# Optimization experiments

Measured on AMD Instinct MI355X. Metric: run time of the kernel, lower is better.

The kernel has to match this reference:

```python
import jax, jax.numpy as jnp
import numpy as np

N_NODES = 100000
N_EDGES = 1600000
IN_DIM, HID, EMB = 128, 128, 128
NUM_EDGE_FEAT = 3
BN_EPS = 1e-5


def _lin(key, fan_in, fan_out):
    k1, k2 = jax.random.split(key)
    lim = 1.0 / np.sqrt(fan_in)
    W = jax.random.uniform(k1, (fan_in, fan_out), minval=-lim, maxval=lim, dtype=jnp.float32)
    b = jax.random.uniform(k2, (fan_out,), minval=-lim, maxval=lim, dtype=jnp.float32)
    return W, b


def setup_inputs() -> dict:
    key = jax.random.key(0)
    ks = jax.random.split(key, 12)
    x = jax.random.normal(ks[0], (N_NODES, IN_DIM), dtype=jnp.float32)
    edge_index = jax.random.randint(ks[1], (2, N_EDGES), 0, N_NODES, dtype=jnp.int32)
    edge_attr = jax.random.normal(ks[2], (N_EDGES, NUM_EDGE_FEAT), dtype=jnp.float32)
    params = {}
    dims = [(IN_DIM, HID), (HID, HID), (HID, HID)]
    for i, (fi, fo) in enumerate(dims, 1):
        W, b = _lin(ks[2 + i], fi, fo)
        We, be = _lin(ks[5 + i], NUM_EDGE_FEAT, fo)
        params[f'W{i}'] = W; params[f'b{i}'] = b
        params[f'We{i}'] = We; params[f'be{i}'] = be
        params[f'g{i}'] = jnp.ones((fo,), jnp.float32)
        params[f'bt{i}'] = jnp.zeros((fo,), jnp.float32)
    Wl, bl = _lin(ks[9], HID, EMB)
    params['Wl'] = Wl; params['bl'] = bl
    return {'x': x, 'edge_index': edge_index, 'edge_attr': edge_attr, **params}


def _gcn_conv(x, row, col, edge_attr, W, b, We, be):
    h = x @ W + b                    # [N, d]
    e = edge_attr @ We + be          # [E, d]
    n = x.shape[0]
    deg = jax.ops.segment_sum(jnp.ones_like(row, dtype=h.dtype), row, num_segments=n) + 1.0
    dinv = deg ** -0.5               # deg >= 1, never inf
    norm = dinv[row] * dinv[col]     # [E]
    msg = norm[:, None] * jax.nn.relu(h[row] + e)  # gather + fused elementwise
    return jax.ops.segment_sum(msg, col, num_segments=n)  # scatter-add to targets


def _bn(x, g, bt):
    m = jnp.mean(x, axis=0)
    v = jnp.mean((x - m) ** 2, axis=0)  # biased var (training-mode batchnorm)
    return (x - m) * jax.lax.rsqrt(v + BN_EPS) * g + bt


def reference(x, edge_index, edge_attr,
              W1, b1, We1, be1, g1, bt1,
              W2, b2, We2, be2, g2, bt2,
              W3, b3, We3, be3, g3, bt3,
              Wl, bl):
    row, col = edge_index[0], edge_index[1]
    h = jax.nn.relu(_gcn_conv(x, row, col, edge_attr, W1, b1, We1, be1))
    h = _bn(h, g1, bt1)
    h = jax.nn.relu(_gcn_conv(h, row, col, edge_attr, W2, b2, We2, be2))
    h = _bn(h, g2, bt2)
    h = jax.nn.relu(_gcn_conv(h, row, col, edge_attr, W3, b3, We3, be3))
    h = _bn(h, g3, bt3)
    return h @ Wl + bl
```

## Files before the change

### kernel.cpp

```cpp
#include <hip/hip_runtime.h>
#include <stdint.h>

#define NN 100000
#define NE 1600000
#define DIM 128
#define BN_EPS 1e-5f
#define NBUCK 391
#define NBLK_GEMM 1563
#define NBLK_AGG 6250
#define NB_HIST 512
#define CSR_PAD 32
#define NREP 64

typedef unsigned int uint;
typedef unsigned short ushort;
typedef unsigned char uchar;
typedef __attribute__((ext_vector_type(8))) short short8;
typedef __attribute__((ext_vector_type(4))) float f32x4;
typedef __attribute__((ext_vector_type(2))) float v2f;


static __device__ __forceinline__ ushort f2bf(float f) {
    uint u = __float_as_uint(f);
    u += 0x7FFF + ((u >> 16) & 1);
    return (ushort)(u >> 16);
}
static __device__ __forceinline__ float bf_lo(uint p) { return __uint_as_float(p << 16); }
static __device__ __forceinline__ float bf_hi(uint p) { return __uint_as_float(p & 0xFFFF0000u); }

static __device__ __forceinline__ v2f vfma(v2f a, v2f b, v2f c) {
    return __builtin_elementwise_fma(a, b, c);
}
static __device__ __forceinline__ v2f vbc(float s) { v2f r = {s, s}; return r; }


__global__ __launch_bounds__(256) void k_count(const int* __restrict__ ei,
                                               int* __restrict__ rowCnt,
                                               int* __restrict__ colCnt) {
    __shared__ int hr[NBUCK], hc[NBUCK];
    int tid = threadIdx.x;
    for (int b = tid; b < NBUCK; b += 256) { hr[b] = 0; hc[b] = 0; }
    __syncthreads();
    const int gstep = NB_HIST * 256;
    const int gt = blockIdx.x * 256 + tid;
    for (int e = gt; e < NE; e += gstep) {
        atomicAdd(&hr[ei[e] >> 8], 1);
        atomicAdd(&hc[ei[NE + e] >> 8], 1);
    }
    __syncthreads();
    for (int b = tid; b < NBUCK; b += 256) {
        if (hr[b]) atomicAdd(&rowCnt[b], hr[b]);
        if (hc[b]) atomicAdd(&colCnt[b], hc[b]);
    }
}

__global__ __launch_bounds__(512) void k_scanb(const int* __restrict__ rowCnt,
                                               const int* __restrict__ colCnt,
                                               int* __restrict__ rowBase,
                                               int* __restrict__ colBase,
                                               int* __restrict__ rowCur,
                                               int* __restrict__ colCur) {
    __shared__ int s[512];
    int tid = threadIdx.x;
    int v = (tid < NBUCK) ? rowCnt[tid] : 0;
    s[tid] = v;
    __syncthreads();
    for (int d = 1; d < 512; d <<= 1) {
        int a = (tid >= d) ? s[tid - d] : 0;
        __syncthreads();
        s[tid] += a;
        __syncthreads();
    }
    if (tid < NBUCK) { int e = s[tid] - v; rowBase[tid] = e; rowCur[tid] = e; }
    if (tid == NBUCK) rowBase[NBUCK] = s[NBUCK];
    __syncthreads();
    v = (tid < NBUCK) ? colCnt[tid] : 0;
    s[tid] = v;
    __syncthreads();
    for (int d = 1; d < 512; d <<= 1) {
        int a = (tid >= d) ? s[tid - d] : 0;
        __syncthreads();
        s[tid] += a;
        __syncthreads();
    }
    if (tid < NBUCK) { int e = s[tid] - v; colBase[tid] = e; colCur[tid] = e; }
    if (tid == NBUCK) colBase[NBUCK] = s[NBUCK];
}

__global__ __launch_bounds__(256) void k_scat(const int* __restrict__ ei,
                                              const float* __restrict__ ea,
                                              int* __restrict__ rowCur,
                                              int* __restrict__ colCur,
                                              uchar* __restrict__ rowScat,
                                              uint4* __restrict__ tmp) {
    __shared__ int hr[NBUCK], hc[NBUCK], lbr[NBUCK], lbc[NBUCK], lcr[NBUCK], lcc[NBUCK];
    int tid = threadIdx.x;
    for (int b = tid; b < NBUCK; b += 256) { hr[b] = 0; hc[b] = 0; lcr[b] = 0; lcc[b] = 0; }
    __syncthreads();
    const int gstep = NB_HIST * 256;
    const int gt = blockIdx.x * 256 + tid;
    for (int e = gt; e < NE; e += gstep) {
        atomicAdd(&hr[ei[e] >> 8], 1);
        atomicAdd(&hc[ei[NE + e] >> 8], 1);
    }
    __syncthreads();
    for (int b = tid; b < NBUCK; b += 256) {
        lbr[b] = hr[b] ? atomicAdd(&rowCur[b], hr[b]) : 0;
        lbc[b] = hc[b] ? atomicAdd(&colCur[b], hc[b]) : 0;
    }
    __syncthreads();
    for (int e = gt; e < NE; e += gstep) {
        int r = ei[e];
        int c = ei[NE + e];
        int posr = lbr[r >> 8] + atomicAdd(&lcr[r >> 8], 1);
        rowScat[posr] = (uchar)(r & 255);
        float3 eav = *(const float3*)&ea[(size_t)e * 3];
        uint4 rec;
        rec.x = 0u;
        rec.y = ((uint)f2bf(eav.x) << 16) | (uint)f2bf(eav.y);
        rec.z = ((uint)f2bf(eav.z) << 16) | (uint)(c & 255);
        rec.w = (uint)r;
        int posc = lbc[c >> 8] + atomicAdd(&lcc[c >> 8], 1);
        tmp[posc] = rec;
    }
}

__global__ __launch_bounds__(1024) void k_deg(const uchar* __restrict__ rowScat,
                                              const int* __restrict__ rowBase,
                                              float* __restrict__ dinv) {
    __shared__ int h[256];
    int tid = threadIdx.x;
    int b = blockIdx.x;
    if (tid < 256) h[tid] = 0;
    __syncthreads();
    int base = rowBase[b], cnt = rowBase[b + 1] - base;
    for (int i = tid; i < cnt; i += 1024) atomicAdd(&h[rowScat[base + i]], 1);
    __syncthreads();
    if (tid < 256) {
        int node = b * 256 + tid;
        if (node < NN) dinv[node] = rsqrtf((float)h[tid] + 1.0f);
    }
}

__global__ __launch_bounds__(1024) void k_sort_col(const uint4* __restrict__ tmp,
                                                   const int* __restrict__ colBase,
                                                   const float* __restrict__ dinv,
                                                   uint4* __restrict__ csr,
                                                   int* __restrict__ offs) {
    __shared__ int hh[256], sc[256], cur[256];
    __shared__ float dloc[256];
    int tid = threadIdx.x;
    int b = blockIdx.x;
    if (tid < 256) {
        hh[tid] = 0;
        int node = b * 256 + tid;
        dloc[tid] = (node < NN) ? dinv[node] : 0.0f;
    }
    __syncthreads();
    int base = colBase[b], cnt = colBase[b + 1] - base;
    for (int i = tid; i < cnt; i += 1024) atomicAdd(&hh[tmp[base + i].z & 255], 1);
    __syncthreads();
    int v = 0;
    if (tid < 256) { v = hh[tid]; sc[tid] = v; }
    __syncthreads();
    for (int d = 1; d < 256; d <<= 1) {
        int add = 0;
        if (tid < 256 && tid >= d) add = sc[tid - d];
        __syncthreads();
        if (tid < 256) sc[tid] += add;
        __syncthreads();
    }
    if (tid < 256) {
        int excl = sc[tid] - v;
        int node = b * 256 + tid;
        if (node < NN) offs[node] = base + excl;
        if (b == NBUCK - 1 && tid == 0) offs[NN] = NE;
        cur[tid] = excl;
    }
    __syncthreads();
    for (int i = tid; i < cnt; i += 1024) {
        uint4 rec = tmp[base + i];
        int f = rec.z & 255;
        rec.x = __float_as_uint(dinv[(int)rec.w] * dloc[f]);
        int pos = atomicAdd(&cur[f], 1);
        csr[base + pos] = rec;
    }
}


__global__ __launch_bounds__(128) void k_prep(const float* __restrict__ W,
                                              const float* __restrict__ b,
                                              const float* __restrict__ g,
                                              const float* __restrict__ bt,
                                              const float* __restrict__ sprev,
                                              float* __restrict__ snext,
                                              int mode,
                                              ushort* __restrict__ Wt,
                                              float* __restrict__ beff) {
    __shared__ float s[DIM];
    int k = threadIdx.x;
    if (k < 64) snext[blockIdx.x * 64 + k] = 0.0f;
    float A = 1.0f, B = 0.0f;
    if (mode) {
        float sm = 0.0f, sq = 0.0f;
        for (int r = 0; r < NREP; ++r) {
            sm += sprev[r * 256 + k];
            sq += sprev[r * 256 + 128 + k];
        }
        float m = sm * (1.0f / NN);
        float var = sq * (1.0f / NN) - m * m;
        float rs = rsqrtf(var + BN_EPS);
        A = rs * g[k];
        B = bt[k] - m * A;
    }
    if (blockIdx.x < DIM) {
        int n = blockIdx.x;
        Wt[n * DIM + k] = f2bf(A * W[k * DIM + n]);
    } else {
        int j = blockIdx.x - DIM;
        s[k] = B * W[k * DIM + j];
        __syncthreads();
        for (int d = 64; d > 0; d >>= 1) {
            if (k < d) s[k] += s[k + d];
            __syncthreads();
        }
        if (k == 0) beff[j] = b[j] + s[0];
    }
}


#define GEMM_LANE_SETUP                                                             \
    const int lane = threadIdx.x & 63;                                              \
    const int wv   = threadIdx.x >> 6;                                              \
    const int m    = lane & 15;                                                     \
    const int quad = lane >> 4;                                                     \
    const int row0 = blockIdx.x * 64 + wv * 16;                                     \
    const int rr   = min(row0 + m, NN - 1);

#define GEMM_MFMA_CORE(a0, a1, a2, a3, Wt)                                          \
    f32x4 acc[8];                                                                   \
    _Pragma("unroll")                                                               \
    for (int ft = 0; ft < 8; ++ft) {                                                \
        const short8* bp = (const short8*)&Wt[(size_t)(ft * 16 + m) * DIM + quad * 8]; \
        f32x4 c = {0.f, 0.f, 0.f, 0.f};                                             \
        c = __builtin_amdgcn_mfma_f32_16x16x32_bf16(bp[0],  a0, c, 0, 0, 0);        \
        c = __builtin_amdgcn_mfma_f32_16x16x32_bf16(bp[4],  a1, c, 0, 0, 0);        \
        c = __builtin_amdgcn_mfma_f32_16x16x32_bf16(bp[8],  a2, c, 0, 0, 0);        \
        c = __builtin_amdgcn_mfma_f32_16x16x32_bf16(bp[12], a3, c, 0, 0, 0);        \
        acc[ft] = c;                                                                \
    }                                                                               \
    const int node = row0 + m;

#define GEMM_STORE_BF16(Y)                                                          \
    if (node < NN) {                                                                \
        ushort* yp = &Y[(size_t)node * DIM + quad * 4];                             \
        _Pragma("unroll")                                                           \
        for (int ft = 0; ft < 8; ++ft) {                                            \
            float4 bb = *(const float4*)&beff[ft * 16 + quad * 4];                  \
            ushort4 o = {f2bf(acc[ft][0] + bb.x), f2bf(acc[ft][1] + bb.y),          \
                         f2bf(acc[ft][2] + bb.z), f2bf(acc[ft][3] + bb.w)};         \
            *(ushort4*)&yp[ft * 16] = o;                                            \
        }                                                                           \
    }

static __device__ __forceinline__ short8 cvt8(float4 a, float4 b) {
    short8 r;
    r[0] = (short)f2bf(a.x); r[1] = (short)f2bf(a.y);
    r[2] = (short)f2bf(a.z); r[3] = (short)f2bf(a.w);
    r[4] = (short)f2bf(b.x); r[5] = (short)f2bf(b.y);
    r[6] = (short)f2bf(b.z); r[7] = (short)f2bf(b.w);
    return r;
}

__global__ __launch_bounds__(256) void k_gemm_mf_f32in(const float* __restrict__ Af,
                                                       const ushort* __restrict__ Wt,
                                                       const float* __restrict__ beff,
                                                       ushort* __restrict__ Y) {
    GEMM_LANE_SETUP
    const float4* apf = (const float4*)&Af[(size_t)rr * DIM] + quad * 2;
    short8 a0 = cvt8(apf[0],  apf[1]);
    short8 a1 = cvt8(apf[8],  apf[9]);
    short8 a2 = cvt8(apf[16], apf[17]);
    short8 a3 = cvt8(apf[24], apf[25]);
    GEMM_MFMA_CORE(a0, a1, a2, a3, Wt)
    GEMM_STORE_BF16(Y)
}

__global__ __launch_bounds__(256) void k_gemm_mf_bf(const ushort* __restrict__ Abf,
                                                    const ushort* __restrict__ Wt,
                                                    const float* __restrict__ beff,
                                                    ushort* __restrict__ Y) {
    GEMM_LANE_SETUP
    const short8* ap = (const short8*)&Abf[(size_t)rr * DIM + quad * 8];
    short8 a0 = ap[0];
    short8 a1 = ap[4];
    short8 a2 = ap[8];
    short8 a3 = ap[12];
    GEMM_MFMA_CORE(a0, a1, a2, a3, Wt)
    GEMM_STORE_BF16(Y)
}

__global__ __launch_bounds__(256) void k_gemm_mf_f32(const ushort* __restrict__ Abf,
                                                     const ushort* __restrict__ Wt,
                                                     const float* __restrict__ beff,
                                                     float* __restrict__ Y) {
    GEMM_LANE_SETUP
    const short8* ap = (const short8*)&Abf[(size_t)rr * DIM + quad * 8];
    short8 a0 = ap[0];
    short8 a1 = ap[4];
    short8 a2 = ap[8];
    short8 a3 = ap[12];
    GEMM_MFMA_CORE(a0, a1, a2, a3, Wt)
    if (node < NN) {
        float* yp = &Y[(size_t)node * DIM + quad * 4];
#pragma unroll
        for (int ft = 0; ft < 8; ++ft) {
            float4 bb = *(const float4*)&beff[ft * 16 + quad * 4];
            float4 o = {acc[ft][0] + bb.x, acc[ft][1] + bb.y,
                        acc[ft][2] + bb.z, acc[ft][3] + bb.w};
            *(float4*)&yp[ft * 16] = o;
        }
    }
}


static __device__ __forceinline__ void edge_compute(float4 r, float4 hv, float n,
                                                    const v2f* __restrict__ w0,
                                                    const v2f* __restrict__ w1,
                                                    const v2f* __restrict__ w2,
                                                    const v2f* __restrict__ vbe,
                                                    v2f* __restrict__ acc) {
    uint py = __float_as_uint(r.y), pz = __float_as_uint(r.z);
    v2f va0 = vbc(bf_hi(py)), va1 = vbc(bf_lo(py)), va2 = vbc(bf_hi(pz));
    v2f vn = vbc(n);
    uint hx = __float_as_uint(hv.x), hy = __float_as_uint(hv.y);
    uint hz = __float_as_uint(hv.z), hw = __float_as_uint(hv.w);
    v2f hp[4] = {{bf_lo(hx), bf_hi(hx)}, {bf_lo(hy), bf_hi(hy)},
                 {bf_lo(hz), bf_hi(hz)}, {bf_lo(hw), bf_hi(hw)}};
    const v2f z = {0.0f, 0.0f};
#pragma unroll
    for (int j = 0; j < 4; ++j) {
        v2f e = vfma(va2, w2[j], vbe[j]);
        e = vfma(va1, w1[j], e);
        e = vfma(va0, w0[j], e);
        v2f u = hp[j] + e;
        u = __builtin_elementwise_max(u, z);
        acc[j] = vfma(vn, u, acc[j]);
    }
}

__global__ __launch_bounds__(256) void k_agg(const float4* __restrict__ h4,
                                             const float4* __restrict__ csr,
                                             const int* __restrict__ offs,
                                             const float* __restrict__ We,
                                             const float* __restrict__ be,
                                             uint* __restrict__ tb,
                                             float* __restrict__ stats) {
    __shared__ float pbuf[4][256];
    int wv = threadIdx.x >> 6;
    int lane = threadIdx.x & 63;
    int q  = lane >> 4;
    int oc = lane & 15;
    int j0 = oc * 8;

    float4 t0, t1;
    t0 = *(const float4*)&We[j0];             t1 = *(const float4*)&We[j0 + 4];
    v2f w0[4] = {{t0.x, t0.y}, {t0.z, t0.w}, {t1.x, t1.y}, {t1.z, t1.w}};
    t0 = *(const float4*)&We[DIM + j0];       t1 = *(const float4*)&We[DIM + j0 + 4];
    v2f w1[4] = {{t0.x, t0.y}, {t0.z, t0.w}, {t1.x, t1.y}, {t1.z, t1.w}};
    t0 = *(const float4*)&We[2 * DIM + j0];   t1 = *(const float4*)&We[2 * DIM + j0 + 4];
    v2f w2[4] = {{t0.x, t0.y}, {t0.z, t0.w}, {t1.x, t1.y}, {t1.z, t1.w}};
    t0 = *(const float4*)&be[j0];             t1 = *(const float4*)&be[j0 + 4];
    v2f vbe[4] = {{t0.x, t0.y}, {t0.z, t0.w}, {t1.x, t1.y}, {t1.z, t1.w}};

    v2f smv[4] = {{0,0},{0,0},{0,0},{0,0}};
    v2f sqv[4] = {{0,0},{0,0},{0,0},{0,0}};

    const int v0 = blockIdx.x * 16 + wv * 4;
    int ofs[5];
#pragma unroll
    for (int k = 0; k < 5; ++k) ofs[k] = offs[v0 + k];

    for (int it = 0; it < 4; ++it) {
        int v = v0 + it;
        v2f acc[4] = {{0,0},{0,0},{0,0},{0,0}};
        int s0 = ofs[it], e0 = ofs[it + 1];

        float4 rA1 = csr[s0 + q];
        float4 rA2 = csr[s0 + 4 + q];
        float4 rB1 = csr[s0 + 8 + q];
        float4 rB2 = csr[s0 + 12 + q];
        float4 hA1 = h4[(size_t)__float_as_int(rA1.w) * 16 + oc];
        float4 hA2 = h4[(size_t)__float_as_int(rA2.w) * 16 + oc];

#pragma unroll 2
        for (int base = s0; base < e0; base += 8) {
            float4 hB1 = h4[(size_t)__float_as_int(rB1.w) * 16 + oc];
            float4 hB2 = h4[(size_t)__float_as_int(rB2.w) * 16 + oc];
            float4 rC1 = csr[base + 16 + q];
            float4 rC2 = csr[base + 20 + q];
            float n1 = (base + q < e0) ? rA1.x : 0.0f;
            float n2 = (base + 4 + q < e0) ? rA2.x : 0.0f;
            edge_compute(rA1, hA1, n1, w0, w1, w2, vbe, acc);
            edge_compute(rA2, hA2, n2, w0, w1, w2, vbe, acc);
            rA1 = rB1; rA2 = rB2; rB1 = rC1; rB2 = rC2;
            hA1 = hB1; hA2 = hB2;
        }

#pragma unroll
        for (int j = 0; j < 4; ++j) {
            acc[j].x += __shfl_xor(acc[j].x, 16); acc[j].x += __shfl_xor(acc[j].x, 32);
            acc[j].y += __shfl_xor(acc[j].y, 16); acc[j].y += __shfl_xor(acc[j].y, 32);
        }

        if (q == 0) {
            uint4 pk;
            uint pw[4];
#pragma unroll
            for (int j = 0; j < 4; ++j) {
                acc[j].x = fmaxf(acc[j].x, 0.0f);
                acc[j].y = fmaxf(acc[j].y, 0.0f);
                smv[j] = smv[j] + acc[j];
                sqv[j] = vfma(acc[j], acc[j], sqv[j]);
                pw[j] = ((uint)f2bf(acc[j].y) << 16) | f2bf(acc[j].x);
            }
            pk.x = pw[0]; pk.y = pw[1]; pk.z = pw[2]; pk.w = pw[3];
            *(uint4*)&tb[(size_t)v * 64 + oc * 4] = pk;
        }
    }

    if (q == 0) {
#pragma unroll
        for (int j = 0; j < 4; ++j) {
            pbuf[wv][j0 + 2 * j]       = smv[j].x;
            pbuf[wv][j0 + 2 * j + 1]   = smv[j].y;
            pbuf[wv][128 + j0 + 2 * j]     = sqv[j].x;
            pbuf[wv][128 + j0 + 2 * j + 1] = sqv[j].y;
        }
    }
    __syncthreads();
    int tid = threadIdx.x;
    float s = pbuf[0][tid] + pbuf[1][tid] + pbuf[2][tid] + pbuf[3][tid];
    atomicAdd(&stats[(blockIdx.x & (NREP - 1)) * 256 + tid], s);
}


static inline char* alignp(char* p, size_t a) {
    return (char*)(((uintptr_t)p + a - 1) & ~(uintptr_t)(a - 1));
}

extern "C" void kernel_launch(void* const* d_in, const int* in_sizes, int n_in,
                              void* d_out, int out_size, void* d_ws, size_t ws_size,
                              hipStream_t stream) {
    const float* x   = (const float*)d_in[0];
    const int*   ei  = (const int*)d_in[1];
    const float* ea  = (const float*)d_in[2];
    const float* Wp[3]  = {(const float*)d_in[3],  (const float*)d_in[9],  (const float*)d_in[15]};
    const float* bp[3]  = {(const float*)d_in[4],  (const float*)d_in[10], (const float*)d_in[16]};
    const float* Wep[3] = {(const float*)d_in[5],  (const float*)d_in[11], (const float*)d_in[17]};
    const float* bep[3] = {(const float*)d_in[6],  (const float*)d_in[12], (const float*)d_in[18]};
    const float* gp[3]  = {(const float*)d_in[7],  (const float*)d_in[13], (const float*)d_in[19]};
    const float* btp[3] = {(const float*)d_in[8],  (const float*)d_in[14], (const float*)d_in[20]};
    const float* Wl  = (const float*)d_in[21];
    const float* bl  = (const float*)d_in[22];
    float* out = (float*)d_out;

    char* p = (char*)d_ws;
    auto alloc = [&](size_t bytes) -> void* {
        p = alignp(p, 256);
        void* r = (void*)p;
        p += bytes;
        return r;
    };

    int*    bcnt     = (int*)alloc(2 * NBUCK * sizeof(int));
    int*    rowCnt   = bcnt;
    int*    colCnt   = bcnt + NBUCK;
    int*    rowBase  = (int*)alloc((NBUCK + 1) * sizeof(int));
    int*    colBase  = (int*)alloc((NBUCK + 1) * sizeof(int));
    int*    rowCur   = (int*)alloc(NBUCK * sizeof(int));
    int*    colCur   = (int*)alloc(NBUCK * sizeof(int));
    int*    offs     = (int*)alloc((NN + 1) * sizeof(int));
    float*  dinv     = (float*)alloc(NN * sizeof(float));
    uchar*  rowScat  = (uchar*)alloc(NE * sizeof(uchar));
    uint4*  csr      = (uint4*)alloc(((size_t)NE + CSR_PAD) * sizeof(uint4));
    ushort* h_bf     = (ushort*)alloc((size_t)NN * DIM * sizeof(ushort));
    ushort* t_bf     = (ushort*)alloc((size_t)NN * DIM * sizeof(ushort));
    ushort* Wt       = (ushort*)alloc(DIM * DIM * sizeof(ushort));
    float*  beff     = (float*)alloc(DIM * sizeof(float));
    float*  sb0      = (float*)alloc((size_t)NREP * 256 * sizeof(float));
    float*  sb1      = (float*)alloc((size_t)NREP * 256 * sizeof(float));

    uint4* tmp = (uint4*)t_bf;

    hipMemsetAsync(bcnt, 0, 2 * NBUCK * sizeof(int), stream);
    hipMemsetAsync(csr + NE, 0, CSR_PAD * sizeof(uint4), stream);
    k_count<<<NB_HIST, 256, 0, stream>>>(ei, rowCnt, colCnt);
    k_scanb<<<1, 512, 0, stream>>>(rowCnt, colCnt, rowBase, colBase, rowCur, colCur);
    k_scat<<<NB_HIST, 256, 0, stream>>>(ei, ea, rowCur, colCur, rowScat, tmp);
    k_deg<<<NBUCK, 1024, 0, stream>>>(rowScat, rowBase, dinv);
    k_sort_col<<<NBUCK, 1024, 0, stream>>>(tmp, colBase, dinv, csr, offs);

    float* sbs[2] = {sb0, sb1};
    for (int l = 0; l < 3; ++l) {
        float* scur = sbs[l & 1];
        float* sprev = sbs[(l + 1) & 1];
        const float* gg = (l == 0) ? gp[0] : gp[l - 1];
        const float* bb = (l == 0) ? btp[0] : btp[l - 1];
        k_prep<<<256, 128, 0, stream>>>(Wp[l], bp[l], gg, bb, sprev, scur,
                                        (l == 0) ? 0 : 1, Wt, beff);
        if (l == 0)
            k_gemm_mf_f32in<<<NBLK_GEMM, 256, 0, stream>>>(x, Wt, beff, h_bf);
        else
            k_gemm_mf_bf<<<NBLK_GEMM, 256, 0, stream>>>(t_bf, Wt, beff, h_bf);
        k_agg<<<NBLK_AGG, 256, 0, stream>>>((const float4*)h_bf, (const float4*)csr, offs,
                                            Wep[l], bep[l], (uint*)t_bf, scur);
    }

    k_prep<<<256, 128, 0, stream>>>(Wl, bl, gp[2], btp[2], sb0, sb1, 1, Wt, beff);
    k_gemm_mf_f32<<<NBLK_GEMM, 256, 0, stream>>>(t_bf, Wt, beff, out);
}
```

Measured before the change: 679.9 us.

## Fold BN-affine weight prep into GEMM prologue and trim setup kernels

Drops the separate k_prep launch: every GEMM block now recomputes the BN-folded bf16 transposed weights and effective bias into padded LDS, then reads B operands from LDS. The CSR pad memset moves into k_scanb, and a separate byte array of fine column indices lets k_sort_col build its histogram without re-reading 16-byte records. This saves launches and global traffic but makes each of ~1563 blocks read the full 64KB fp32 W and the BN stats buffers redundantly, which adds per-block latency and LDS pressure (~35KB+) that may reduce occupancy.

```diff
diff --git a/kernel.cpp b/kernel.cpp
--- a/kernel.cpp
+++ b/kernel.cpp
@@ -11,6 +11,7 @@
 #define NB_HIST 512
 #define CSR_PAD 32
 #define NREP 64
+#define WTL_STRIDE 136
 
 typedef unsigned int uint;
 typedef unsigned short ushort;
@@ -59,9 +60,11 @@
                                                int* __restrict__ rowBase,
                                                int* __restrict__ colBase,
                                                int* __restrict__ rowCur,
-                                               int* __restrict__ colCur) {
+                                               int* __restrict__ colCur,
+                                               uint4* __restrict__ csr) {
     __shared__ int s[512];
     int tid = threadIdx.x;
+    if (tid < CSR_PAD * 4) ((uint*)(csr + NE))[tid] = 0u;
     int v = (tid < NBUCK) ? rowCnt[tid] : 0;
     s[tid] = v;
     __syncthreads();
@@ -92,6 +95,7 @@
                                               int* __restrict__ rowCur,
                                               int* __restrict__ colCur,
                                               uchar* __restrict__ rowScat,
+                                              uchar* __restrict__ colFine,
                                               uint4* __restrict__ tmp) {
     __shared__ int hr[NBUCK], hc[NBUCK], lbr[NBUCK], lbc[NBUCK], lcr[NBUCK], lcc[NBUCK];
     int tid = threadIdx.x;
@@ -122,6 +126,7 @@
         rec.w = (uint)r;
         int posc = lbc[c >> 8] + atomicAdd(&lcc[c >> 8], 1);
         tmp[posc] = rec;
+        colFine[posc] = (uchar)(c & 255);
     }
 }
 
@@ -143,6 +148,7 @@
 }
 
 __global__ __launch_bounds__(1024) void k_sort_col(const uint4* __restrict__ tmp,
+                                                   const uchar* __restrict__ colFine,
                                                    const int* __restrict__ colBase,
                                                    const float* __restrict__ dinv,
                                                    uint4* __restrict__ csr,
@@ -158,7 +164,7 @@
     }
     __syncthreads();
     int base = colBase[b], cnt = colBase[b + 1] - base;
-    for (int i = tid; i < cnt; i += 1024) atomicAdd(&hh[tmp[base + i].z & 255], 1);
+    for (int i = tid; i < cnt; i += 1024) atomicAdd(&hh[colFine[base + i]], 1);
     __syncthreads();
     int v = 0;
     if (tid < 256) { v = hh[tid]; sc[tid] = v; }
@@ -188,46 +194,47 @@
 }
 
 
-__global__ __launch_bounds__(128) void k_prep(const float* __restrict__ W,
-                                              const float* __restrict__ b,
-                                              const float* __restrict__ g,
-                                              const float* __restrict__ bt,
-                                              const float* __restrict__ sprev,
-                                              float* __restrict__ snext,
-                                              int mode,
-                                              ushort* __restrict__ Wt,
-                                              float* __restrict__ beff) {
-    __shared__ float s[DIM];
-    int k = threadIdx.x;
-    if (k < 64) snext[blockIdx.x * 64 + k] = 0.0f;
-    float A = 1.0f, B = 0.0f;
-    if (mode) {
-        float sm = 0.0f, sq = 0.0f;
-        for (int r = 0; r < NREP; ++r) {
-            sm += sprev[r * 256 + k];
-            sq += sprev[r * 256 + 128 + k];
-        }
-        float m = sm * (1.0f / NN);
-        float var = sq * (1.0f / NN) - m * m;
-        float rs = rsqrtf(var + BN_EPS);
-        A = rs * g[k];
-        B = bt[k] - m * A;
-    }
-    if (blockIdx.x < DIM) {
-        int n = blockIdx.x;
-        Wt[n * DIM + k] = f2bf(A * W[k * DIM + n]);
-    } else {
-        int j = blockIdx.x - DIM;
-        s[k] = B * W[k * DIM + j];
-        __syncthreads();
-        for (int d = 64; d > 0; d >>= 1) {
-            if (k < d) s[k] += s[k + d];
-            __syncthreads();
-        }
-        if (k == 0) beff[j] = b[j] + s[0];
-    }
-}
-
+#define GEMM_FOLD_PROLOGUE                                                          \
+    __shared__ ushort WtL[DIM * WTL_STRIDE];                                        \
+    __shared__ float beffL[DIM];                                                    \
+    __shared__ float ABs[2 * DIM];                                                  \
+    __shared__ float bred[256];                                                     \
+    {                                                                               \
+        int tid = threadIdx.x;                                                      \
+        if (blockIdx.x < 256 && tid < 64) snext[blockIdx.x * 64 + tid] = 0.0f;      \
+        if (tid < DIM) {                                                            \
+            float A = 1.0f, B = 0.0f;                                               \
+            if (mode) {                                                             \
+                float sm = 0.0f, sq = 0.0f;                                         \
+                for (int r = 0; r < NREP; ++r) {                                    \
+                    sm += sprev[r * 256 + tid];                                     \
+                    sq += sprev[r * 256 + 128 + tid];                               \
+                }                                                                   \
+                float mm = sm * (1.0f / NN);                                        \
+                float var = sq * (1.0f / NN) - mm * mm;                             \
+                float rs = rsqrtf(var + BN_EPS);                                    \
+                A = rs * g[tid];                                                    \
+                B = bt[tid] - mm * A;                                               \
+            }                                                                       \
+            ABs[tid] = A; ABs[DIM + tid] = B;                                       \
+        }                                                                           \
+        __syncthreads();                                                            \
+        int n = tid & 127;                                                          \
+        int k0 = (tid >> 7) * 64;                                                   \
+        float bacc = 0.0f;                                                          \
+        for (int kk = 0; kk < 64; kk += 2) {                                        \
+            int k = k0 + kk;                                                        \
+            float w0v = W[(size_t)k * DIM + n];                                     \
+            float w1v = W[(size_t)(k + 1) * DIM + n];                               \
+            bacc += ABs[DIM + k] * w0v + ABs[DIM + k + 1] * w1v;                    \
+            uint pack = ((uint)f2bf(ABs[k + 1] * w1v) << 16) | (uint)f2bf(ABs[k] * w0v); \
+            *(uint*)((char*)WtL + (size_t)n * 272 + (size_t)k * 2) = pack;          \
+        }                                                                           \
+        bred[tid] = bacc;                                                           \
+        __syncthreads();                                                            \
+        if (tid < DIM) beffL[tid] = bvec[tid] + bred[tid] + bred[tid + DIM];        \
+        __syncthreads();                                                            \
+    }
 
 #define GEMM_LANE_SETUP                                                             \
     const int lane = threadIdx.x & 63;                                              \
@@ -237,16 +244,19 @@
     const int row0 = blockIdx.x * 64 + wv * 16;                                     \
     const int rr   = min(row0 + m, NN - 1);
 
-#define GEMM_MFMA_CORE(a0, a1, a2, a3, Wt)                                          \
+#define GEMM_MFMA_CORE(a0, a1, a2, a3)                                              \
     f32x4 acc[8];                                                                   \
     _Pragma("unroll")                                                               \
     for (int ft = 0; ft < 8; ++ft) {                                                \
-        const short8* bp = (const short8*)&Wt[(size_t)(ft * 16 + m) * DIM + quad * 8]; \
+        const short8* bp = (const short8*)((const char*)WtL + (size_t)(ft * 16 + m) * 272 + quad * 16); \
+        const short8* bq = (const short8*)((const char*)WtL + (size_t)(ft * 16 + m) * 272 + 64 + quad * 16); \
+        const short8* br = (const short8*)((const char*)WtL + (size_t)(ft * 16 + m) * 272 + 128 + quad * 16); \
+        const short8* bs = (const short8*)((const char*)WtL + (size_t)(ft * 16 + m) * 272 + 192 + quad * 16); \
         f32x4 c = {0.f, 0.f, 0.f, 0.f};                                             \
-        c = __builtin_amdgcn_mfma_f32_16x16x32_bf16(bp[0],  a0, c, 0, 0, 0);        \
-        c = __builtin_amdgcn_mfma_f32_16x16x32_bf16(bp[4],  a1, c, 0, 0, 0);        \
-        c = __builtin_amdgcn_mfma_f32_16x16x32_bf16(bp[8],  a2, c, 0, 0, 0);        \
-        c = __builtin_amdgcn_mfma_f32_16x16x32_bf16(bp[12], a3, c, 0, 0, 0);        \
+        c = __builtin_amdgcn_mfma_f32_16x16x32_bf16(bp[0], a0, c, 0, 0, 0);         \
+        c = __builtin_amdgcn_mfma_f32_16x16x32_bf16(bq[0], a1, c, 0, 0, 0);         \
+        c = __builtin_amdgcn_mfma_f32_16x16x32_bf16(br[0], a2, c, 0, 0, 0);         \
+        c = __builtin_amdgcn_mfma_f32_16x16x32_bf16(bs[0], a3, c, 0, 0, 0);         \
         acc[ft] = c;                                                                \
     }                                                                               \
     const int node = row0 + m;
@@ -256,7 +266,7 @@
         ushort* yp = &Y[(size_t)node * DIM + quad * 4];                             \
         _Pragma("unroll")                                                           \
         for (int ft = 0; ft < 8; ++ft) {                                            \
-            float4 bb = *(const float4*)&beff[ft * 16 + quad * 4];                  \
+            float4 bb = *(const float4*)&beffL[ft * 16 + quad * 4];                 \
             ushort4 o = {f2bf(acc[ft][0] + bb.x), f2bf(acc[ft][1] + bb.y),          \
                          f2bf(acc[ft][2] + bb.z), f2bf(acc[ft][3] + bb.w)};         \
             *(ushort4*)&yp[ft * 16] = o;                                            \
@@ -272,50 +282,68 @@
     return r;
 }
 
-__global__ __launch_bounds__(256) void k_gemm_mf_f32in(const float* __restrict__ Af,
-                                                       const ushort* __restrict__ Wt,
-                                                       const float* __restrict__ beff,
-                                                       ushort* __restrict__ Y) {
+__global__ __launch_bounds__(256) void k_gemm_f32in(const float* __restrict__ Af,
+                                                    const float* __restrict__ W,
+                                                    const float* __restrict__ bvec,
+                                                    const float* __restrict__ g,
+                                                    const float* __restrict__ bt,
+                                                    const float* __restrict__ sprev,
+                                                    float* __restrict__ snext,
+                                                    int mode,
+                                                    ushort* __restrict__ Y) {
+    GEMM_FOLD_PROLOGUE
     GEMM_LANE_SETUP
     const float4* apf = (const float4*)&Af[(size_t)rr * DIM] + quad * 2;
     short8 a0 = cvt8(apf[0],  apf[1]);
     short8 a1 = cvt8(apf[8],  apf[9]);
     short8 a2 = cvt8(apf[16], apf[17]);
     short8 a3 = cvt8(apf[24], apf[25]);
-    GEMM_MFMA_CORE(a0, a1, a2, a3, Wt)
+    GEMM_MFMA_CORE(a0, a1, a2, a3)
     GEMM_STORE_BF16(Y)
 }
 
-__global__ __launch_bounds__(256) void k_gemm_mf_bf(const ushort* __restrict__ Abf,
-                                                    const ushort* __restrict__ Wt,
-                                                    const float* __restrict__ beff,
-                                                    ushort* __restrict__ Y) {
+__global__ __launch_bounds__(256) void k_gemm_bf(const ushort* __restrict__ Abf,
+                                                 const float* __restrict__ W,
+                                                 const float* __restrict__ bvec,
+                                                 const float* __restrict__ g,
+                                                 const float* __restrict__ bt,
+                                                 const float* __restrict__ sprev,
+                                                 float* __restrict__ snext,
+                                                 int mode,
+                                                 ushort* __restrict__ Y) {
+    GEMM_FOLD_PROLOGUE
     GEMM_LANE_SETUP
     const short8* ap = (const short8*)&Abf[(size_t)rr * DIM + quad * 8];
     short8 a0 = ap[0];
     short8 a1 = ap[4];
     short8 a2 = ap[8];
     short8 a3 = ap[12];
-    GEMM_MFMA_CORE(a0, a1, a2, a3, Wt)
+    GEMM_MFMA_CORE(a0, a1, a2, a3)
     GEMM_STORE_BF16(Y)
 }
 
-__global__ __launch_bounds__(256) void k_gemm_mf_f32(const ushort* __restrict__ Abf,
-                                                     const ushort* __restrict__ Wt,
-                                                     const float* __restrict__ beff,
+__global__ __launch_bounds__(256) void k_gemm_f32out(const ushort* __restrict__ Abf,
+                                                     const float* __restrict__ W,
+                                                     const float* __restrict__ bvec,
+                                                     const float* __restrict__ g,
+                                                     const float* __restrict__ bt,
+                                                     const float* __restrict__ sprev,
+                                                     float* __restrict__ snext,
+                                                     int mode,
                                                      float* __restrict__ Y) {
+    GEMM_FOLD_PROLOGUE
     GEMM_LANE_SETUP
     const short8* ap = (const short8*)&Abf[(size_t)rr * DIM + quad * 8];
     short8 a0 = ap[0];
     short8 a1 = ap[4];
     short8 a2 = ap[8];
     short8 a3 = ap[12];
-    GEMM_MFMA_CORE(a0, a1, a2, a3, Wt)
+    GEMM_MFMA_CORE(a0, a1, a2, a3)
     if (node < NN) {
         float* yp = &Y[(size_t)node * DIM + quad * 4];
 #pragma unroll
         for (int ft = 0; ft < 8; ++ft) {
-            float4 bb = *(const float4*)&beff[ft * 16 + quad * 4];
+            float4 bb = *(const float4*)&beffL[ft * 16 + quad * 4];
             float4 o = {acc[ft][0] + bb.x, acc[ft][1] + bb.y,
                         acc[ft][2] + bb.z, acc[ft][3] + bb.w};
             *(float4*)&yp[ft * 16] = o;
@@ -483,23 +511,21 @@
     int*    offs     = (int*)alloc((NN + 1) * sizeof(int));
     float*  dinv     = (float*)alloc(NN * sizeof(float));
     uchar*  rowScat  = (uchar*)alloc(NE * sizeof(uchar));
+    uchar*  colFine  = (uchar*)alloc(NE * sizeof(uchar));
     uint4*  csr      = (uint4*)alloc(((size_t)NE + CSR_PAD) * sizeof(uint4));
     ushort* h_bf     = (ushort*)alloc((size_t)NN * DIM * sizeof(ushort));
     ushort* t_bf     = (ushort*)alloc((size_t)NN * DIM * sizeof(ushort));
-    ushort* Wt       = (ushort*)alloc(DIM * DIM * sizeof(ushort));
-    float*  beff     = (float*)alloc(DIM * sizeof(float));
     float*  sb0      = (float*)alloc((size_t)NREP * 256 * sizeof(float));
     float*  sb1      = (float*)alloc((size_t)NREP * 256 * sizeof(float));
 
     uint4* tmp = (uint4*)t_bf;
 
     hipMemsetAsync(bcnt, 0, 2 * NBUCK * sizeof(int), stream);
-    hipMemsetAsync(csr + NE, 0, CSR_PAD * sizeof(uint4), stream);
     k_count<<<NB_HIST, 256, 0, stream>>>(ei, rowCnt, colCnt);
-    k_scanb<<<1, 512, 0, stream>>>(rowCnt, colCnt, rowBase, colBase, rowCur, colCur);
-    k_scat<<<NB_HIST, 256, 0, stream>>>(ei, ea, rowCur, colCur, rowScat, tmp);
+    k_scanb<<<1, 512, 0, stream>>>(rowCnt, colCnt, rowBase, colBase, rowCur, colCur, csr);
+    k_scat<<<NB_HIST, 256, 0, stream>>>(ei, ea, rowCur, colCur, rowScat, colFine, tmp);
     k_deg<<<NBUCK, 1024, 0, stream>>>(rowScat, rowBase, dinv);
-    k_sort_col<<<NBUCK, 1024, 0, stream>>>(tmp, colBase, dinv, csr, offs);
+    k_sort_col<<<NBUCK, 1024, 0, stream>>>(tmp, colFine, colBase, dinv, csr, offs);
 
     float* sbs[2] = {sb0, sb1};
     for (int l = 0; l < 3; ++l) {
@@ -507,16 +533,16 @@
         float* sprev = sbs[(l + 1) & 1];
         const float* gg = (l == 0) ? gp[0] : gp[l - 1];
         const float* bb = (l == 0) ? btp[0] : btp[l - 1];
-        k_prep<<<256, 128, 0, stream>>>(Wp[l], bp[l], gg, bb, sprev, scur,
-                                        (l == 0) ? 0 : 1, Wt, beff);
         if (l == 0)
-            k_gemm_mf_f32in<<<NBLK_GEMM, 256, 0, stream>>>(x, Wt, beff, h_bf);
+            k_gemm_f32in<<<NBLK_GEMM, 256, 0, stream>>>(x, Wp[0], bp[0], gg, bb,
+                                                        sprev, scur, 0, h_bf);
         else
-            k_gemm_mf_bf<<<NBLK_GEMM, 256, 0, stream>>>(t_bf, Wt, beff, h_bf);
+            k_gemm_bf<<<NBLK_GEMM, 256, 0, stream>>>(t_bf, Wp[l], bp[l], gg, bb,
+                                                     sprev, scur, 1, h_bf);
         k_agg<<<NBLK_AGG, 256, 0, stream>>>((const float4*)h_bf, (const float4*)csr, offs,
                                             Wep[l], bep[l], (uint*)t_bf, scur);
     }
 
-    k_prep<<<256, 128, 0, stream>>>(Wl, bl, gp[2], btp[2], sb0, sb1, 1, Wt, beff);
-    k_gemm_mf_f32<<<NBLK_GEMM, 256, 0, stream>>>(t_bf, Wt, beff, out);
-}
+    k_gemm_f32out<<<NBLK_GEMM, 256, 0, stream>>>(t_bf, Wl, bl, gp[2], btp[2],
+                                                 sb0, sb1, 1, out);
+}
```

Measured after the change: 623.6 us. -8.3%, faster.
